# Kernel optimization log

Measured on AMD Instinct MI355X. Metric: run time of the kernel, lower is better.

## Reference

```python
import jax, jax.numpy as jnp
import numpy as np

N = 2048      # number of ROIs
C = 1024      # in_channels == inter_channels
G = 16        # groups
D = C // G    # per-group dim = 64


def _bbox_overlaps(b1, b2):
    # mmdet-1.x IoU with +1 pixel convention; b1:(N,4), b2:(M,4)
    area1 = (b1[:, 2] - b1[:, 0] + 1) * (b1[:, 3] - b1[:, 1] + 1)  # (N,)
    area2 = (b2[:, 2] - b2[:, 0] + 1) * (b2[:, 3] - b2[:, 1] + 1)  # (M,)
    lt = jnp.maximum(b1[:, None, :2], b2[None, :, :2])             # (N,M,2)
    rb = jnp.minimum(b1[:, None, 2:], b2[None, :, 2:])             # (N,M,2)
    wh = jnp.clip(rb - lt + 1, 0)
    inter = wh[..., 0] * wh[..., 1]                                # (N,M)
    return inter / (area1[:, None] + area2[None, :] - inter)


def setup_inputs() -> dict:
    key = jax.random.key(0)
    ks = jax.random.split(key, 9)
    in_x = jax.random.normal(ks[0], (N, C), dtype=jnp.float32)
    # valid boxes: [batch_idx, x1, y1, x2, y2]
    xy = jax.random.uniform(ks[1], (N, 2), minval=0.0, maxval=800.0)
    wh = jax.random.uniform(ks[2], (N, 2), minval=8.0, maxval=200.0)
    rois = jnp.concatenate([jnp.zeros((N, 1)), xy, xy + wh], axis=1).astype(jnp.float32)
    s = 1.0 / np.sqrt(C)
    W0 = jax.random.normal(ks[3], (C, C), dtype=jnp.float32) * s
    b0 = jnp.zeros((C,), dtype=jnp.float32)
    W1 = jax.random.normal(ks[4], (C, C), dtype=jnp.float32) * s
    b1 = jnp.zeros((C,), dtype=jnp.float32)
    # grouped 1x1 conv: per group maps C channels -> D channels
    Wout = jax.random.normal(ks[5], (G, D, C), dtype=jnp.float32) * s
    bout = jnp.zeros((C,), dtype=jnp.float32)
    return {"in_x": in_x, "rois": rois, "W0": W0, "b0": b0, "W1": W1,
            "b1": b1, "Wout": Wout, "bout": bout}


def reference(in_x, rois, W0, b0, W1, b1, Wout, bout):
    # self-attention path: in_ref_x = in_x, ref_rois = rois
    # embed convs are pre-activation (relu -> 1x1 conv), shared for x and ref_x
    def embed(v):
        v = jax.nn.relu(v) @ W0.T + b0
        v = jax.nn.relu(v) @ W1.T + b1
        return v
    x = embed(in_x)                      # (N, C)
    ref_x = x                            # shared convs, same input
    xg = x.reshape(N, G, D)
    rg = ref_x.reshape(N, G, D)
    scores = jnp.einsum('ngd,mgd->ngm', xg, rg) / jnp.sqrt(jnp.float32(D))  # (N,G,N)
    ious = _bbox_overlaps(rois[:, 1:], rois[:, 1:])                          # (N,N)
    scores = scores + jnp.log(ious[:, None, :] + 1e-6)
    attn = jax.nn.softmax(scores, axis=2)                                    # (N,G,N)
    y = jnp.einsum('ngm,mc->ngc', attn, in_x)                                # (N,G,C)
    out = jnp.einsum('ngc,goc->ngo', y, Wout).reshape(N, C) + bout           # (N,C)
    return out
```

## Files before the change

kernel.cpp:

```cpp
#include <hip/hip_runtime.h>
#include <math.h>

constexpr int NROI = 2048;
constexpr int CDIM = 1024;
constexpr int NG   = 16;
constexpr int DH   = 64;

typedef __attribute__((ext_vector_type(8))) short short8;
typedef __attribute__((ext_vector_type(4))) float floatx4;

#define MFMA_BF16(a, b, c) __builtin_amdgcn_mfma_f32_16x16x32_bf16((a), (b), (c), 0, 0, 0)

__device__ __forceinline__ short f2bf(float f) {
  unsigned u = __float_as_uint(f);
  unsigned r = 0x7fffu + ((u >> 16) & 1u);
  return (short)((u + r) >> 16);
}
__device__ __forceinline__ short f2bf_rtz(float f) {
  return (short)(__float_as_uint(f) >> 16);
}
__device__ __forceinline__ unsigned pack2(float a, float b) {
  return (unsigned)(unsigned short)f2bf(a) | ((unsigned)(unsigned short)f2bf(b) << 16);
}

typedef __attribute__((address_space(1))) void GV;
typedef __attribute__((address_space(3))) void LV;
__device__ __forceinline__ void gl2lds16(const void* g, void* l) {
  __builtin_amdgcn_global_load_lds((GV*)g, (LV*)l, 16, 0, 0);
}

__device__ __forceinline__ short8 brelu(short8 v) {
  union { short8 s; unsigned u[4]; } x; x.s = v;
#pragma unroll
  for (int i = 0; i < 4; ++i) {
    unsigned m = (x.u[i] >> 15) & 0x10001u;
    x.u[i] &= ~(m * 0xFFFFu);
  }
  return x.s;
}

__global__ __launch_bounds__(256) void conv_iou(
    const float* __restrict__ in_x, const float* __restrict__ W0,
    const float* __restrict__ W1, const float* __restrict__ Wout,
    const float* __restrict__ rois,
    short* __restrict__ xin_b, short* __restrict__ W0b,
    short* __restrict__ W1b, short* __restrict__ Woutb,
    unsigned short* __restrict__ biasln)
{
  const int b = blockIdx.x;
  if (b < 2048) {
    const int i = b * 256 + threadIdx.x;
    {
      const float4 v = ((const float4*)in_x)[i];
      uint2 u; u.x = pack2(v.x, v.y); u.y = pack2(v.z, v.w);
      ((uint2*)xin_b)[i] = u;
    }
    if (i < 262144) {
      float4 v = ((const float4*)W0)[i];
      uint2 u; u.x = pack2(v.x, v.y); u.y = pack2(v.z, v.w);
      ((uint2*)W0b)[i] = u;
      v = ((const float4*)W1)[i];
      u.x = pack2(v.x, v.y); u.y = pack2(v.z, v.w);
      ((uint2*)W1b)[i] = u;
      v = ((const float4*)Wout)[i];
      u.x = pack2(v.x, v.y); u.y = pack2(v.z, v.w);
      ((uint2*)Woutb)[i] = u;
    }
  } else {
    const int p = (b - 2048) * 256 + threadIdx.x;
    const int q = p >> 11, k = p & 2047;
    const float qx1 = rois[q * 5 + 1], qy1 = rois[q * 5 + 2];
    const float qx2 = rois[q * 5 + 3], qy2 = rois[q * 5 + 4];
    const float qa = (qx2 - qx1 + 1.f) * (qy2 - qy1 + 1.f);
    const float kx1 = rois[k * 5 + 1], ky1 = rois[k * 5 + 2];
    const float kx2 = rois[k * 5 + 3], ky2 = rois[k * 5 + 4];
    const float ka = (kx2 - kx1 + 1.f) * (ky2 - ky1 + 1.f);
    float iw = fminf(qx2, kx2) - fmaxf(qx1, kx1) + 1.f;
    float ih = fminf(qy2, ky2) - fmaxf(qy1, ky1) + 1.f;
    iw = fmaxf(iw, 0.f); ih = fmaxf(ih, 0.f);
    const float inter = iw * ih;
    const float iou = inter / (qa + ka - inter);
    biasln[p] = (unsigned short)f2bf(__logf(iou + 1e-6f));
  }
}

__global__ __launch_bounds__(256) void gemm128(
    const short* __restrict__ A, const short* __restrict__ BW0,
    const short* __restrict__ BWout, const float* __restrict__ b0,
    short* __restrict__ t0b, short* __restrict__ zT)
{
  __shared__ short As[16 * 512];
  __shared__ short Bs[16 * 512];
  const int t = threadIdx.x, w = t >> 6, lane = t & 63;
  const int wm = w >> 1, wn = w & 1;
  const int row0 = blockIdx.y * 128;
  const int col0g = blockIdx.x * 128;
  const int isW0 = col0g < 1024;
  const short* B = isW0 ? BW0 : BWout;
  const int col0 = col0g & 1023;
  const int srow = lane & 15, skq = (lane >> 4) * 8;

  floatx4 acc[4][4];
#pragma unroll
  for (int i = 0; i < 4; ++i)
#pragma unroll
    for (int j = 0; j < 4; ++j) acc[i][j] = (floatx4){0.f, 0.f, 0.f, 0.f};

  for (int k0 = 0; k0 < CDIM; k0 += 64) {
    __syncthreads();
#pragma unroll
    for (int q = 0; q < 4; ++q) {
      const int f = w * 4 + q, rt = f >> 1, kh = f & 1;
      gl2lds16(A + (size_t)(row0 + rt * 16 + srow) * CDIM + k0 + kh * 32 + skq,
               &As[f * 512]);
      gl2lds16(B + (size_t)(col0 + rt * 16 + srow) * CDIM + k0 + kh * 32 + skq,
               &Bs[f * 512]);
    }
    __syncthreads();
#pragma unroll
    for (int kh = 0; kh < 2; ++kh) {
      short8 a[4], bf[4];
#pragma unroll
      for (int i = 0; i < 4; ++i) {
        a[i] = *(const short8*)&As[(((wm * 4 + i) * 2) + kh) * 512 + lane * 8];
        if (isW0) a[i] = brelu(a[i]);
      }
#pragma unroll
      for (int j = 0; j < 4; ++j)
        bf[j] = *(const short8*)&Bs[(((wn * 4 + j) * 2) + kh) * 512 + lane * 8];
#pragma unroll
      for (int i = 0; i < 4; ++i)
#pragma unroll
        for (int j = 0; j < 4; ++j)
          acc[i][j] = MFMA_BF16(a[i], bf[j], acc[i][j]);
    }
  }

  const int colL = lane & 15, qq = lane >> 4;
  if (isW0) {
    float bj[4];
#pragma unroll
    for (int j = 0; j < 4; ++j) bj[j] = b0[col0 + wn * 64 + j * 16 + colL];
#pragma unroll
    for (int i = 0; i < 4; ++i)
#pragma unroll
      for (int j = 0; j < 4; ++j)
#pragma unroll
        for (int r = 0; r < 4; ++r) {
          const int row = row0 + wm * 64 + i * 16 + qq * 4 + r;
          const int cc  = col0 + wn * 64 + j * 16 + colL;
          t0b[(size_t)row * CDIM + cc] = f2bf(acc[i][j][r] + bj[j]);
        }
  } else {
#pragma unroll
    for (int i = 0; i < 4; ++i)
#pragma unroll
      for (int j = 0; j < 4; ++j) {
        unsigned long long u = 0;
#pragma unroll
        for (int r = 0; r < 4; ++r)
          u |= ((unsigned long long)(unsigned short)f2bf(acc[i][j][r])) << (16 * r);
        const int cc  = col0 + wn * 64 + j * 16 + colL;
        const int row = row0 + wm * 64 + i * 16 + qq * 4;
        *(unsigned long long*)&zT[(size_t)cc * NROI + row] = u;
      }
  }
}

__global__ __launch_bounds__(256) void gemm_relu_nt(
    const short* __restrict__ A, const short* __restrict__ B,
    const float* __restrict__ bias, short* __restrict__ C)
{
  __shared__ short As[8 * 512];
  __shared__ short Bs[8 * 512];
  const int t = threadIdx.x, w = t >> 6, lane = t & 63;
  const int wm = w >> 1, wn = w & 1;
  const int row0 = blockIdx.y * 64, col0 = blockIdx.x * 64;
  const int rlo = lane & 15, khi = (lane >> 4) * 8;

  floatx4 acc[2][2];
#pragma unroll
  for (int i = 0; i < 2; ++i)
#pragma unroll
    for (int j = 0; j < 2; ++j) acc[i][j] = (floatx4){0.f, 0.f, 0.f, 0.f};

  for (int k0 = 0; k0 < CDIM; k0 += 64) {
    __syncthreads();
#pragma unroll
    for (int kh = 0; kh < 2; ++kh) {
      gl2lds16(A + (size_t)(row0 + w * 16 + rlo) * CDIM + k0 + kh * 32 + khi,
               &As[(w * 2 + kh) * 512]);
      gl2lds16(B + (size_t)(col0 + w * 16 + rlo) * CDIM + k0 + kh * 32 + khi,
               &Bs[(w * 2 + kh) * 512]);
    }
    __syncthreads();
#pragma unroll
    for (int kh = 0; kh < 2; ++kh) {
      short8 a0 = *(const short8*)&As[((wm * 2 + 0) * 2 + kh) * 512 + lane * 8];
      short8 a1 = *(const short8*)&As[((wm * 2 + 1) * 2 + kh) * 512 + lane * 8];
      a0 = brelu(a0); a1 = brelu(a1);
      const short8 b0f = *(const short8*)&Bs[((wn * 2 + 0) * 2 + kh) * 512 + lane * 8];
      const short8 b1f = *(const short8*)&Bs[((wn * 2 + 1) * 2 + kh) * 512 + lane * 8];
      acc[0][0] = MFMA_BF16(a0, b0f, acc[0][0]);
      acc[0][1] = MFMA_BF16(a0, b1f, acc[0][1]);
      acc[1][0] = MFMA_BF16(a1, b0f, acc[1][0]);
      acc[1][1] = MFMA_BF16(a1, b1f, acc[1][1]);
    }
  }

  const int colL = lane & 15, qq = lane >> 4;
  float bj[2];
  bj[0] = bias[col0 + wn * 32 + colL];
  bj[1] = bias[col0 + wn * 32 + 16 + colL];
#pragma unroll
  for (int i = 0; i < 2; ++i)
#pragma unroll
    for (int j = 0; j < 2; ++j)
#pragma unroll
      for (int r = 0; r < 4; ++r) {
        const int row = row0 + wm * 32 + i * 16 + qq * 4 + r;
        const int cc  = col0 + wn * 32 + j * 16 + colL;
        C[(size_t)row * CDIM + cc] = f2bf(acc[i][j][r] + bj[j]);
      }
}

__global__ __launch_bounds__(512) void attn_ln(
    const short* __restrict__ Xb,
    const short* __restrict__ ZTb,
    const unsigned short* __restrict__ biasln,
    const float* __restrict__ bout,
    float* __restrict__ Out)
{
  const int g  = blockIdx.y;
  const int n0 = blockIdx.x * 128;
  const int t = threadIdx.x, w = t >> 6, lane = t & 63;
  const int col = lane & 15, qq = lane >> 4;
  const int t16 = (w >> 1) * 16, h32 = (w & 1) * 32;
  const int rlo = lane & 15, khi = (lane >> 4) * 8;

  __shared__ short Kf[2][8 * 512];
  __shared__ short Vf[2][8 * 512];
  __shared__ short Pf[8 * 1024];

  const size_t qoff = (size_t)(n0 + w * 16 + col) * CDIM + g * DH;
  const short8 qf0 = *(const short8*)(Xb + qoff + qq * 8);
  const short8 qf1 = *(const short8*)(Xb + qoff + 32 + qq * 8);

  floatx4 oc[4];
#pragma unroll
  for (int dt = 0; dt < 4; ++dt) oc[dt] = (floatx4){0.f, 0.f, 0.f, 0.f};
  float lsum[4] = {0.f, 0.f, 0.f, 0.f};

  const int qrow0 = n0 + w * 16 + qq * 4;

  uint2 bbc[4], bbn[4];
#pragma unroll
  for (int ct = 0; ct < 4; ++ct)
    bbc[ct] = *(const uint2*)(biasln + (size_t)(ct * 16 + col) * NROI + qrow0);

  gl2lds16(Xb + (size_t)(t16 + rlo) * CDIM + g * DH + h32 + khi, &Kf[0][w * 512]);
  gl2lds16(ZTb + (size_t)(g * DH + t16 + rlo) * NROI + h32 + khi, &Vf[0][w * 512]);
  __syncthreads();

  for (int it = 0; it < NROI / 64; ++it) {
    const int p = it & 1;
    const int m0 = it * 64;
    if (it + 1 < NROI / 64) {
      const int m1 = m0 + 64;
      gl2lds16(Xb + (size_t)(m1 + t16 + rlo) * CDIM + g * DH + h32 + khi,
               &Kf[1 - p][w * 512]);
      gl2lds16(ZTb + (size_t)(g * DH + t16 + rlo) * NROI + m1 + h32 + khi,
               &Vf[1 - p][w * 512]);
#pragma unroll
      for (int ct = 0; ct < 4; ++ct)
        bbn[ct] = *(const uint2*)(biasln + (size_t)(m1 + ct * 16 + col) * NROI + qrow0);
    }

    floatx4 sc[4];
#pragma unroll
    for (int ct = 0; ct < 4; ++ct) {
      const short8 b0 = *(const short8*)&Kf[p][(ct * 2 + 0) * 512 + lane * 8];
      const short8 b1 = *(const short8*)&Kf[p][(ct * 2 + 1) * 512 + lane * 8];
      floatx4 z4 = (floatx4){0.f, 0.f, 0.f, 0.f};
      z4 = MFMA_BF16(qf0, b0, z4);
      z4 = MFMA_BF16(qf1, b1, z4);
      sc[ct] = z4;
    }

#pragma unroll
    for (int ct = 0; ct < 4; ++ct) {
      const unsigned ux = bbc[ct].x, uy = bbc[ct].y;
      sc[ct][0] = __expf(fmaf(sc[ct][0], 0.125f, __uint_as_float(ux << 16)));
      sc[ct][1] = __expf(fmaf(sc[ct][1], 0.125f, __uint_as_float(ux & 0xFFFF0000u)));
      sc[ct][2] = __expf(fmaf(sc[ct][2], 0.125f, __uint_as_float(uy << 16)));
      sc[ct][3] = __expf(fmaf(sc[ct][3], 0.125f, __uint_as_float(uy & 0xFFFF0000u)));
    }
#pragma unroll
    for (int r = 0; r < 4; ++r)
      lsum[r] += sc[0][r] + sc[1][r] + sc[2][r] + sc[3][r];

    {
      short* pw = &Pf[w * 1024];
#pragma unroll
      for (int ct = 0; ct < 4; ++ct) {
        const int key = ct * 16 + col;
        const int base = (key >> 5) * 512 + (key & 7);
#pragma unroll
        for (int r = 0; r < 4; ++r) {
          const int dl = (4 * qq + r) + ((key >> 3) & 3) * 16;
          pw[base + dl * 8] = f2bf_rtz(sc[ct][r]);
        }
      }
      const short8 pa0 = *(const short8*)&pw[0 * 512 + lane * 8];
      const short8 pa1 = *(const short8*)&pw[1 * 512 + lane * 8];
#pragma unroll
      for (int dt = 0; dt < 4; ++dt) {
        const short8 v0 = *(const short8*)&Vf[p][(dt * 2 + 0) * 512 + lane * 8];
        const short8 v1 = *(const short8*)&Vf[p][(dt * 2 + 1) * 512 + lane * 8];
        oc[dt] = MFMA_BF16(pa0, v0, oc[dt]);
        oc[dt] = MFMA_BF16(pa1, v1, oc[dt]);
      }
    }
    __syncthreads();
#pragma unroll
    for (int ct = 0; ct < 4; ++ct) bbc[ct] = bbn[ct];
  }

#pragma unroll
  for (int r = 0; r < 4; ++r) {
    float s = lsum[r];
    s += __shfl_xor(s, 1); s += __shfl_xor(s, 2);
    s += __shfl_xor(s, 4); s += __shfl_xor(s, 8);
    lsum[r] = s;
  }
#pragma unroll
  for (int dt = 0; dt < 4; ++dt) {
    const float bo = bout[g * DH + dt * 16 + col];
#pragma unroll
    for (int r = 0; r < 4; ++r)
      Out[(size_t)(qrow0 + r) * CDIM + g * DH + dt * 16 + col] =
          oc[dt][r] / lsum[r] + bo;
  }
}

extern "C" void kernel_launch(void* const* d_in, const int* in_sizes, int n_in,
                              void* d_out, int out_size, void* d_ws, size_t ws_size,
                              hipStream_t stream) {
  const float* in_x = (const float*)d_in[0];
  const float* rois = (const float*)d_in[1];
  const float* W0   = (const float*)d_in[2];
  const float* b0   = (const float*)d_in[3];
  const float* W1   = (const float*)d_in[4];
  const float* b1   = (const float*)d_in[5];
  const float* Wout = (const float*)d_in[6];
  const float* bout = (const float*)d_in[7];
  char* w8 = (char*)d_ws;

  short* xin_b = (short*)w8;
  short* W0b   = (short*)(w8 + ((size_t)4 << 20));
  short* W1b   = (short*)(w8 + ((size_t)6 << 20));
  short* Woutb = (short*)(w8 + ((size_t)8 << 20));
  short* zT    = (short*)(w8 + ((size_t)10 << 20));
  unsigned short* biasln = (unsigned short*)(w8 + ((size_t)14 << 20));
  short* xb  = xin_b;
  short* t0b = (short*)d_out;

  conv_iou<<<2048 + 16384, 256, 0, stream>>>(in_x, W0, W1, Wout, rois,
                                             xin_b, W0b, W1b, Woutb, biasln);
  gemm128<<<dim3(16, 16), 256, 0, stream>>>(xin_b, W0b, Woutb, b0, t0b, zT);
  gemm_relu_nt<<<dim3(16, 32), 256, 0, stream>>>(t0b, W1b, b1, xb);
  attn_ln<<<dim3(NROI / 128, NG), 512, 0, stream>>>(xb, zT, biasln, bout,
                                                    (float*)d_out);
}
```

Baseline: 205.5 us.

## Double-buffer GEMMs, split IoU kernel, and multiply attention by IoU instead of log-add

Separates the bf16 conversion from the IoU computation and vectorises IoU into four keys per thread, storing iou+eps rather than its log. Both embedding GEMMs gain double-buffered LDS prefetch, and the second GEMM uses larger 128x64 tiles. The attention kernel now computes exp(score)*iou, which removes a log per pair, but loads the bias per element from row-major storage without prefetching, which may add memory latency in the hot loop. P rounding changes from truncation to round-to-nearest.

```diff
diff --git a/kernel.cpp b/kernel.cpp
--- a/kernel.cpp
+++ b/kernel.cpp
@@ -16,8 +16,8 @@
   unsigned r = 0x7fffu + ((u >> 16) & 1u);
   return (short)((u + r) >> 16);
 }
-__device__ __forceinline__ short f2bf_rtz(float f) {
-  return (short)(__float_as_uint(f) >> 16);
+__device__ __forceinline__ float bf2f(unsigned short u) {
+  return __uint_as_float(((unsigned)u) << 16);
 }
 __device__ __forceinline__ unsigned pack2(float a, float b) {
   return (unsigned)(unsigned short)f2bf(a) | ((unsigned)(unsigned short)f2bf(b) << 16);
@@ -39,39 +39,43 @@
   return x.s;
 }
 
-__global__ __launch_bounds__(256) void conv_iou(
+__global__ __launch_bounds__(256) void convert_kernel(
     const float* __restrict__ in_x, const float* __restrict__ W0,
     const float* __restrict__ W1, const float* __restrict__ Wout,
-    const float* __restrict__ rois,
     short* __restrict__ xin_b, short* __restrict__ W0b,
-    short* __restrict__ W1b, short* __restrict__ Woutb,
-    unsigned short* __restrict__ biasln)
+    short* __restrict__ W1b, short* __restrict__ Woutb)
 {
-  const int b = blockIdx.x;
-  if (b < 2048) {
-    const int i = b * 256 + threadIdx.x;
-    {
-      const float4 v = ((const float4*)in_x)[i];
-      uint2 u; u.x = pack2(v.x, v.y); u.y = pack2(v.z, v.w);
-      ((uint2*)xin_b)[i] = u;
-    }
-    if (i < 262144) {
-      float4 v = ((const float4*)W0)[i];
-      uint2 u; u.x = pack2(v.x, v.y); u.y = pack2(v.z, v.w);
-      ((uint2*)W0b)[i] = u;
-      v = ((const float4*)W1)[i];
-      u.x = pack2(v.x, v.y); u.y = pack2(v.z, v.w);
-      ((uint2*)W1b)[i] = u;
-      v = ((const float4*)Wout)[i];
-      u.x = pack2(v.x, v.y); u.y = pack2(v.z, v.w);
-      ((uint2*)Woutb)[i] = u;
-    }
-  } else {
-    const int p = (b - 2048) * 256 + threadIdx.x;
-    const int q = p >> 11, k = p & 2047;
-    const float qx1 = rois[q * 5 + 1], qy1 = rois[q * 5 + 2];
-    const float qx2 = rois[q * 5 + 3], qy2 = rois[q * 5 + 4];
-    const float qa = (qx2 - qx1 + 1.f) * (qy2 - qy1 + 1.f);
+  const int i = blockIdx.x * 256 + threadIdx.x;
+  {
+    const float4 v = ((const float4*)in_x)[i];
+    uint2 u; u.x = pack2(v.x, v.y); u.y = pack2(v.z, v.w);
+    ((uint2*)xin_b)[i] = u;
+  }
+  if (i < 262144) {
+    float4 v = ((const float4*)W0)[i];
+    uint2 u; u.x = pack2(v.x, v.y); u.y = pack2(v.z, v.w);
+    ((uint2*)W0b)[i] = u;
+    v = ((const float4*)W1)[i];
+    u.x = pack2(v.x, v.y); u.y = pack2(v.z, v.w);
+    ((uint2*)W1b)[i] = u;
+    v = ((const float4*)Wout)[i];
+    u.x = pack2(v.x, v.y); u.y = pack2(v.z, v.w);
+    ((uint2*)Woutb)[i] = u;
+  }
+}
+
+__global__ __launch_bounds__(256) void iou4_kernel(const float* __restrict__ rois,
+                                                   unsigned short* __restrict__ biasb)
+{
+  const int q  = blockIdx.y;
+  const int k0 = (blockIdx.x * 256 + threadIdx.x) * 4;
+  const float qx1 = rois[q * 5 + 1], qy1 = rois[q * 5 + 2];
+  const float qx2 = rois[q * 5 + 3], qy2 = rois[q * 5 + 4];
+  const float qa = (qx2 - qx1 + 1.f) * (qy2 - qy1 + 1.f);
+  float v[4];
+#pragma unroll
+  for (int j = 0; j < 4; ++j) {
+    const int k = k0 + j;
     const float kx1 = rois[k * 5 + 1], ky1 = rois[k * 5 + 2];
     const float kx2 = rois[k * 5 + 3], ky2 = rois[k * 5 + 4];
     const float ka = (kx2 - kx1 + 1.f) * (ky2 - ky1 + 1.f);
@@ -79,26 +83,27 @@
     float ih = fminf(qy2, ky2) - fmaxf(qy1, ky1) + 1.f;
     iw = fmaxf(iw, 0.f); ih = fmaxf(ih, 0.f);
     const float inter = iw * ih;
-    const float iou = inter / (qa + ka - inter);
-    biasln[p] = (unsigned short)f2bf(__logf(iou + 1e-6f));
-  }
-}
-
-__global__ __launch_bounds__(256) void gemm128(
+    v[j] = inter * __builtin_amdgcn_rcpf(qa + ka - inter) + 1e-6f;
+  }
+  uint2 u; u.x = pack2(v[0], v[1]); u.y = pack2(v[2], v[3]);
+  *(uint2*)&biasb[(size_t)q * NROI + k0] = u;
+}
+
+__global__ __launch_bounds__(256) void gemm_fused(
     const short* __restrict__ A, const short* __restrict__ BW0,
     const short* __restrict__ BWout, const float* __restrict__ b0,
     short* __restrict__ t0b, short* __restrict__ zT)
 {
-  __shared__ short As[16 * 512];
-  __shared__ short Bs[16 * 512];
+  __shared__ short As[2][16 * 512];
+  __shared__ short Bs[2][16 * 512];
   const int t = threadIdx.x, w = t >> 6, lane = t & 63;
   const int wm = w >> 1, wn = w & 1;
   const int row0 = blockIdx.y * 128;
-  const int col0g = blockIdx.x * 128;
-  const int isW0 = col0g < 1024;
+  const int bx = blockIdx.x;
+  const bool isW0 = bx < 8;
+  const int col0 = (bx & 7) * 128;
   const short* B = isW0 ? BW0 : BWout;
-  const int col0 = col0g & 1023;
-  const int srow = lane & 15, skq = (lane >> 4) * 8;
+  const int rlo = lane & 15, khi = (lane >> 4) * 8;
 
   floatx4 acc[4][4];
 #pragma unroll
@@ -106,34 +111,45 @@
 #pragma unroll
     for (int j = 0; j < 4; ++j) acc[i][j] = (floatx4){0.f, 0.f, 0.f, 0.f};
 
-  for (int k0 = 0; k0 < CDIM; k0 += 64) {
-    __syncthreads();
-#pragma unroll
-    for (int q = 0; q < 4; ++q) {
-      const int f = w * 4 + q, rt = f >> 1, kh = f & 1;
-      gl2lds16(A + (size_t)(row0 + rt * 16 + srow) * CDIM + k0 + kh * 32 + skq,
-               &As[f * 512]);
-      gl2lds16(B + (size_t)(col0 + rt * 16 + srow) * CDIM + k0 + kh * 32 + skq,
-               &Bs[f * 512]);
-    }
-    __syncthreads();
+#pragma unroll
+  for (int q = 0; q < 4; ++q) {
+    const int f = w * 4 + q, rt = f >> 1, kh = f & 1;
+    gl2lds16(A + (size_t)(row0 + rt * 16 + rlo) * CDIM + kh * 32 + khi, &As[0][f * 512]);
+    gl2lds16(B + (size_t)(col0 + rt * 16 + rlo) * CDIM + kh * 32 + khi, &Bs[0][f * 512]);
+  }
+  __syncthreads();
+
+  for (int it = 0; it < 16; ++it) {
+    const int p = it & 1;
+    if (it < 15) {
+      const int k1 = (it + 1) * 64;
+#pragma unroll
+      for (int q = 0; q < 4; ++q) {
+        const int f = w * 4 + q, rt = f >> 1, kh = f & 1;
+        gl2lds16(A + (size_t)(row0 + rt * 16 + rlo) * CDIM + k1 + kh * 32 + khi,
+                 &As[1 - p][f * 512]);
+        gl2lds16(B + (size_t)(col0 + rt * 16 + rlo) * CDIM + k1 + kh * 32 + khi,
+                 &Bs[1 - p][f * 512]);
+      }
+    }
 #pragma unroll
     for (int kh = 0; kh < 2; ++kh) {
       short8 a[4], bf[4];
 #pragma unroll
       for (int i = 0; i < 4; ++i) {
-        a[i] = *(const short8*)&As[(((wm * 4 + i) * 2) + kh) * 512 + lane * 8];
+        a[i] = *(const short8*)&As[p][((wm * 4 + i) * 2 + kh) * 512 + lane * 8];
         if (isW0) a[i] = brelu(a[i]);
       }
 #pragma unroll
       for (int j = 0; j < 4; ++j)
-        bf[j] = *(const short8*)&Bs[(((wn * 4 + j) * 2) + kh) * 512 + lane * 8];
+        bf[j] = *(const short8*)&Bs[p][((wn * 4 + j) * 2 + kh) * 512 + lane * 8];
 #pragma unroll
       for (int i = 0; i < 4; ++i)
 #pragma unroll
         for (int j = 0; j < 4; ++j)
           acc[i][j] = MFMA_BF16(a[i], bf[j], acc[i][j]);
     }
+    __syncthreads();
   }
 
   const int colL = lane & 15, qq = lane >> 4;
@@ -156,10 +172,9 @@
     for (int i = 0; i < 4; ++i)
 #pragma unroll
       for (int j = 0; j < 4; ++j) {
-        unsigned long long u = 0;
-#pragma unroll
-        for (int r = 0; r < 4; ++r)
-          u |= ((unsigned long long)(unsigned short)f2bf(acc[i][j][r])) << (16 * r);
+        unsigned long long u =
+            (unsigned long long)pack2(acc[i][j][0], acc[i][j][1]) |
+            ((unsigned long long)pack2(acc[i][j][2], acc[i][j][3]) << 32);
         const int cc  = col0 + wn * 64 + j * 16 + colL;
         const int row = row0 + wm * 64 + i * 16 + qq * 4;
         *(unsigned long long*)&zT[(size_t)cc * NROI + row] = u;
@@ -167,45 +182,68 @@
   }
 }
 
-__global__ __launch_bounds__(256) void gemm_relu_nt(
+__global__ __launch_bounds__(256) void gemm1k(
     const short* __restrict__ A, const short* __restrict__ B,
     const float* __restrict__ bias, short* __restrict__ C)
 {
-  __shared__ short As[8 * 512];
-  __shared__ short Bs[8 * 512];
+  __shared__ short As[2][16 * 512];
+  __shared__ short Bs[2][8 * 512];
   const int t = threadIdx.x, w = t >> 6, lane = t & 63;
   const int wm = w >> 1, wn = w & 1;
-  const int row0 = blockIdx.y * 64, col0 = blockIdx.x * 64;
+  const int row0 = blockIdx.y * 128, col0 = blockIdx.x * 64;
   const int rlo = lane & 15, khi = (lane >> 4) * 8;
 
-  floatx4 acc[2][2];
-#pragma unroll
-  for (int i = 0; i < 2; ++i)
+  floatx4 acc[4][2];
+#pragma unroll
+  for (int i = 0; i < 4; ++i)
 #pragma unroll
     for (int j = 0; j < 2; ++j) acc[i][j] = (floatx4){0.f, 0.f, 0.f, 0.f};
 
-  for (int k0 = 0; k0 < CDIM; k0 += 64) {
+#pragma unroll
+  for (int q = 0; q < 4; ++q) {
+    const int f = w * 4 + q, rt = f >> 1, kh = f & 1;
+    gl2lds16(A + (size_t)(row0 + rt * 16 + rlo) * CDIM + kh * 32 + khi, &As[0][f * 512]);
+  }
+#pragma unroll
+  for (int q = 0; q < 2; ++q) {
+    const int f = w * 2 + q, rt = f >> 1, kh = f & 1;
+    gl2lds16(B + (size_t)(col0 + rt * 16 + rlo) * CDIM + kh * 32 + khi, &Bs[0][f * 512]);
+  }
+  __syncthreads();
+
+  for (int it = 0; it < 16; ++it) {
+    const int p = it & 1;
+    if (it < 15) {
+      const int k1 = (it + 1) * 64;
+#pragma unroll
+      for (int q = 0; q < 4; ++q) {
+        const int f = w * 4 + q, rt = f >> 1, kh = f & 1;
+        gl2lds16(A + (size_t)(row0 + rt * 16 + rlo) * CDIM + k1 + kh * 32 + khi,
+                 &As[1 - p][f * 512]);
+      }
+#pragma unroll
+      for (int q = 0; q < 2; ++q) {
+        const int f = w * 2 + q, rt = f >> 1, kh = f & 1;
+        gl2lds16(B + (size_t)(col0 + rt * 16 + rlo) * CDIM + k1 + kh * 32 + khi,
+                 &Bs[1 - p][f * 512]);
+      }
+    }
+#pragma unroll
+    for (int kh = 0; kh < 2; ++kh) {
+      short8 a[4], bf[2];
+#pragma unroll
+      for (int i = 0; i < 4; ++i)
+        a[i] = brelu(*(const short8*)&As[p][((wm * 4 + i) * 2 + kh) * 512 + lane * 8]);
+#pragma unroll
+      for (int j = 0; j < 2; ++j)
+        bf[j] = *(const short8*)&Bs[p][((wn * 2 + j) * 2 + kh) * 512 + lane * 8];
+#pragma unroll
+      for (int i = 0; i < 4; ++i)
+#pragma unroll
+        for (int j = 0; j < 2; ++j)
+          acc[i][j] = MFMA_BF16(a[i], bf[j], acc[i][j]);
+    }
     __syncthreads();
-#pragma unroll
-    for (int kh = 0; kh < 2; ++kh) {
-      gl2lds16(A + (size_t)(row0 + w * 16 + rlo) * CDIM + k0 + kh * 32 + khi,
-               &As[(w * 2 + kh) * 512]);
-      gl2lds16(B + (size_t)(col0 + w * 16 + rlo) * CDIM + k0 + kh * 32 + khi,
-               &Bs[(w * 2 + kh) * 512]);
-    }
-    __syncthreads();
-#pragma unroll
-    for (int kh = 0; kh < 2; ++kh) {
-      short8 a0 = *(const short8*)&As[((wm * 2 + 0) * 2 + kh) * 512 + lane * 8];
-      short8 a1 = *(const short8*)&As[((wm * 2 + 1) * 2 + kh) * 512 + lane * 8];
-      a0 = brelu(a0); a1 = brelu(a1);
-      const short8 b0f = *(const short8*)&Bs[((wn * 2 + 0) * 2 + kh) * 512 + lane * 8];
-      const short8 b1f = *(const short8*)&Bs[((wn * 2 + 1) * 2 + kh) * 512 + lane * 8];
-      acc[0][0] = MFMA_BF16(a0, b0f, acc[0][0]);
-      acc[0][1] = MFMA_BF16(a0, b1f, acc[0][1]);
-      acc[1][0] = MFMA_BF16(a1, b0f, acc[1][0]);
-      acc[1][1] = MFMA_BF16(a1, b1f, acc[1][1]);
-    }
   }
 
   const int colL = lane & 15, qq = lane >> 4;
@@ -213,29 +251,33 @@
   bj[0] = bias[col0 + wn * 32 + colL];
   bj[1] = bias[col0 + wn * 32 + 16 + colL];
 #pragma unroll
-  for (int i = 0; i < 2; ++i)
+  for (int i = 0; i < 4; ++i)
 #pragma unroll
     for (int j = 0; j < 2; ++j)
 #pragma unroll
       for (int r = 0; r < 4; ++r) {
-        const int row = row0 + wm * 32 + i * 16 + qq * 4 + r;
+        const int row = row0 + wm * 64 + i * 16 + qq * 4 + r;
         const int cc  = col0 + wn * 32 + j * 16 + colL;
         C[(size_t)row * CDIM + cc] = f2bf(acc[i][j][r] + bj[j]);
       }
 }
 
-__global__ __launch_bounds__(512) void attn_ln(
+__global__ __launch_bounds__(512) void attn_bias(
     const short* __restrict__ Xb,
     const short* __restrict__ ZTb,
-    const unsigned short* __restrict__ biasln,
+    const unsigned short* __restrict__ biasb,
     const float* __restrict__ bout,
     float* __restrict__ Out)
 {
   const int g  = blockIdx.y;
   const int n0 = blockIdx.x * 128;
-  const int t = threadIdx.x, w = t >> 6, lane = t & 63;
-  const int col = lane & 15, qq = lane >> 4;
-  const int t16 = (w >> 1) * 16, h32 = (w & 1) * 32;
+  const int t  = threadIdx.x;
+  const int w    = t >> 6;
+  const int lane = t & 63;
+  const int col  = lane & 15;
+  const int qq   = lane >> 4;
+  const int t16 = (w >> 1) * 16;
+  const int h32 = (w & 1) * 32;
   const int rlo = lane & 15, khi = (lane >> 4) * 8;
 
   __shared__ short Kf[2][8 * 512];
@@ -251,19 +293,12 @@
   for (int dt = 0; dt < 4; ++dt) oc[dt] = (floatx4){0.f, 0.f, 0.f, 0.f};
   float lsum[4] = {0.f, 0.f, 0.f, 0.f};
 
-  const int qrow0 = n0 + w * 16 + qq * 4;
-
-  uint2 bbc[4], bbn[4];
-#pragma unroll
-  for (int ct = 0; ct < 4; ++ct)
-    bbc[ct] = *(const uint2*)(biasln + (size_t)(ct * 16 + col) * NROI + qrow0);
-
   gl2lds16(Xb + (size_t)(t16 + rlo) * CDIM + g * DH + h32 + khi, &Kf[0][w * 512]);
   gl2lds16(ZTb + (size_t)(g * DH + t16 + rlo) * NROI + h32 + khi, &Vf[0][w * 512]);
   __syncthreads();
 
   for (int it = 0; it < NROI / 64; ++it) {
-    const int p = it & 1;
+    const int p  = it & 1;
     const int m0 = it * 64;
     if (it + 1 < NROI / 64) {
       const int m1 = m0 + 64;
@@ -271,10 +306,15 @@
                &Kf[1 - p][w * 512]);
       gl2lds16(ZTb + (size_t)(g * DH + t16 + rlo) * NROI + m1 + h32 + khi,
                &Vf[1 - p][w * 512]);
-#pragma unroll
-      for (int ct = 0; ct < 4; ++ct)
-        bbn[ct] = *(const uint2*)(biasln + (size_t)(m1 + ct * 16 + col) * NROI + qrow0);
-    }
+    }
+
+    float bb[4][4];
+#pragma unroll
+    for (int ct = 0; ct < 4; ++ct)
+#pragma unroll
+      for (int r = 0; r < 4; ++r)
+        bb[ct][r] = bf2f(biasb[(size_t)(n0 + w * 16 + qq * 4 + r) * NROI +
+                               m0 + ct * 16 + col]);
 
     floatx4 sc[4];
 #pragma unroll
@@ -288,13 +328,10 @@
     }
 
 #pragma unroll
-    for (int ct = 0; ct < 4; ++ct) {
-      const unsigned ux = bbc[ct].x, uy = bbc[ct].y;
-      sc[ct][0] = __expf(fmaf(sc[ct][0], 0.125f, __uint_as_float(ux << 16)));
-      sc[ct][1] = __expf(fmaf(sc[ct][1], 0.125f, __uint_as_float(ux & 0xFFFF0000u)));
-      sc[ct][2] = __expf(fmaf(sc[ct][2], 0.125f, __uint_as_float(uy << 16)));
-      sc[ct][3] = __expf(fmaf(sc[ct][3], 0.125f, __uint_as_float(uy & 0xFFFF0000u)));
-    }
+    for (int ct = 0; ct < 4; ++ct)
+#pragma unroll
+      for (int r = 0; r < 4; ++r)
+        sc[ct][r] = __expf(sc[ct][r] * 0.125f) * bb[ct][r];
 #pragma unroll
     for (int r = 0; r < 4; ++r)
       lsum[r] += sc[0][r] + sc[1][r] + sc[2][r] + sc[3][r];
@@ -308,7 +345,7 @@
 #pragma unroll
         for (int r = 0; r < 4; ++r) {
           const int dl = (4 * qq + r) + ((key >> 3) & 3) * 16;
-          pw[base + dl * 8] = f2bf_rtz(sc[ct][r]);
+          pw[base + dl * 8] = f2bf(sc[ct][r]);
         }
       }
       const short8 pa0 = *(const short8*)&pw[0 * 512 + lane * 8];
@@ -322,8 +359,6 @@
       }
     }
     __syncthreads();
-#pragma unroll
-    for (int ct = 0; ct < 4; ++ct) bbc[ct] = bbn[ct];
   }
 
 #pragma unroll
@@ -338,7 +373,7 @@
     const float bo = bout[g * DH + dt * 16 + col];
 #pragma unroll
     for (int r = 0; r < 4; ++r)
-      Out[(size_t)(qrow0 + r) * CDIM + g * DH + dt * 16 + col] =
+      Out[(size_t)(n0 + w * 16 + qq * 4 + r) * CDIM + g * DH + dt * 16 + col] =
           oc[dt][r] / lsum[r] + bo;
   }
 }
@@ -361,14 +396,15 @@
   short* W1b   = (short*)(w8 + ((size_t)6 << 20));
   short* Woutb = (short*)(w8 + ((size_t)8 << 20));
   short* zT    = (short*)(w8 + ((size_t)10 << 20));
-  unsigned short* biasln = (unsigned short*)(w8 + ((size_t)14 << 20));
+  unsigned short* biasb = (unsigned short*)(w8 + ((size_t)14 << 20));
   short* xb  = xin_b;
   short* t0b = (short*)d_out;
 
-  conv_iou<<<2048 + 16384, 256, 0, stream>>>(in_x, W0, W1, Wout, rois,
-                                             xin_b, W0b, W1b, Woutb, biasln);
-  gemm128<<<dim3(16, 16), 256, 0, stream>>>(xin_b, W0b, Woutb, b0, t0b, zT);
-  gemm_relu_nt<<<dim3(16, 32), 256, 0, stream>>>(t0b, W1b, b1, xb);
-  attn_ln<<<dim3(NROI / 128, NG), 512, 0, stream>>>(xb, zT, biasln, bout,
-                                                    (float*)d_out);
-}
+  convert_kernel<<<2048, 256, 0, stream>>>(in_x, W0, W1, Wout,
+                                           xin_b, W0b, W1b, Woutb);
+  iou4_kernel<<<dim3(2, NROI), 256, 0, stream>>>(rois, biasb);
+  gemm_fused<<<dim3(16, 16), 256, 0, stream>>>(xin_b, W0b, Woutb, b0, t0b, zT);
+  gemm1k<<<dim3(16, 16), 256, 0, stream>>>(t0b, W1b, b1, xb);
+  attn_bias<<<dim3(NROI / 128, NG), 512, 0, stream>>>(xb, zT, biasb, bout,
+                                                      (float*)d_out);
+}
```

Result: faster. 192.5 us (-6.3%).
